# Kernel tuning notes

Hardware: AMD Instinct MI355X
Metric: run time of the kernel (lower is better)

## Reference

```python
import jax, jax.numpy as jnp
import numpy as np

B, C, L, H, W = 8, 64, 32, 64, 64

def setup_inputs() -> dict:
    key = jax.random.key(0)
    k1, k2, k3, k4, k5 = jax.random.split(key, 5)
    inpt = jax.random.normal(k1, (B, C, L, H, W), dtype=jnp.float32)
    # 1x1x1 conv kernels collapse to per-channel vectors
    theta_w = jax.random.normal(k2, (C,), dtype=jnp.float32) * 0.1  # Conv3d(c,1,1) weight
    g_w = jax.random.normal(k3, (C,), dtype=jnp.float32) * 0.1      # Conv3d(c,1,1) weight
    h_w = jax.random.normal(k4, (C,), dtype=jnp.float32) * 0.1      # Conv3d(1,c,1) weight
    h_b = jax.random.normal(k5, (C,), dtype=jnp.float32) * 0.1      # Conv3d(1,c,1) bias
    return {"inpt": inpt, "theta_w": theta_w, "g_w": g_w, "h_w": h_w, "h_b": h_b}

def reference(inpt, theta_w, g_w, h_w, h_b):
    b, c, l, h, w = inpt.shape
    # theta/g: 1x1x1 convs c->1 == channel contraction
    t = jnp.einsum('bclhw,c->blhw', inpt, theta_w).reshape(b, -1)  # (b, N)
    g = jnp.einsum('bclhw,c->blhw', inpt, g_w).reshape(b, -1)      # (b, N)
    # outer product t[b,1,N]*g[b,N,1] followed by AvgPool1d(N) over last axis
    # == g scaled by mean(t); skip the O(N^2) intermediate entirely
    mt = jnp.mean(t, axis=1, keepdims=True)                        # (b, 1)
    x = (g * mt).reshape(b, 1, l, h, w)
    # h: 1x1x1 conv 1->c with bias
    y = x * h_w[None, :, None, None, None] + h_b[None, :, None, None, None]
    return inpt + y
```

## Files before the change

kernel.cpp:

```cpp
#include <hip/hip_runtime.h>

#define BB 8
#define CC 64
#define NSP 131072
#define N4 32768
#define CHUNKS 128

__global__ __launch_bounds__(256) void k1_gpart(
    const float* __restrict__ inpt, const float* __restrict__ theta_w,
    const float* __restrict__ g_w, float* __restrict__ g_out,
    float* __restrict__ partials, int write_g)
{
    int blk = blockIdx.x;
    int b = blk >> 7;
    int n4 = ((blk & 127) << 8) + threadIdx.x;
    const float4* base = reinterpret_cast<const float4*>(inpt)
                         + (((size_t)b) << 21) + n4;

    float4 t4 = make_float4(0.f, 0.f, 0.f, 0.f);
    float4 g4 = make_float4(0.f, 0.f, 0.f, 0.f);
    #pragma unroll 8
    for (int c = 0; c < CC; ++c) {
        float4 x = base[((size_t)c) << 15];
        float tw = theta_w[c];
        float gw = g_w[c];
        t4.x = fmaf(x.x, tw, t4.x); t4.y = fmaf(x.y, tw, t4.y);
        t4.z = fmaf(x.z, tw, t4.z); t4.w = fmaf(x.w, tw, t4.w);
        g4.x = fmaf(x.x, gw, g4.x); g4.y = fmaf(x.y, gw, g4.y);
        g4.z = fmaf(x.z, gw, g4.z); g4.w = fmaf(x.w, gw, g4.w);
    }
    if (write_g)
        reinterpret_cast<float4*>(g_out)[(((size_t)b) << 15) + n4] = g4;

    float t = (t4.x + t4.y) + (t4.z + t4.w);
    #pragma unroll
    for (int off = 32; off > 0; off >>= 1) t += __shfl_down(t, off);
    __shared__ float red[4];
    int wid = threadIdx.x >> 6;
    if ((threadIdx.x & 63) == 0) red[wid] = t;
    __syncthreads();
    if (threadIdx.x == 0) partials[blk] = (red[0] + red[1]) + (red[2] + red[3]);
}

__global__ __launch_bounds__(512) void k2_mt(
    const float* __restrict__ partials, float* __restrict__ mt)
{
    int b = threadIdx.x >> 6;
    int lane = threadIdx.x & 63;
    float v = partials[(b << 7) + lane] + partials[(b << 7) + 64 + lane];
    #pragma unroll
    for (int off = 32; off > 0; off >>= 1) v += __shfl_down(v, off);
    if (lane == 0) mt[b] = v * (1.0f / (float)NSP);
}

__global__ __launch_bounds__(256) void k3_stream(
    const float* __restrict__ inpt, const float* __restrict__ g,
    const float* __restrict__ mt, const float* __restrict__ h_w,
    const float* __restrict__ h_b, float* __restrict__ out)
{
    size_t i4 = (size_t)blockIdx.x * 256 + threadIdx.x;
    int bc = (int)(i4 >> 15);
    int b = bc >> 6, c = bc & 63;
    float4 x  = reinterpret_cast<const float4*>(inpt)[i4];
    float4 gv = reinterpret_cast<const float4*>(g)[(((size_t)b) << 15) + (i4 & 32767)];
    float s  = mt[b] * h_w[c];
    float hb = h_b[c];
    float4 o;
    o.x = fmaf(gv.x, s, x.x + hb);
    o.y = fmaf(gv.y, s, x.y + hb);
    o.z = fmaf(gv.z, s, x.z + hb);
    o.w = fmaf(gv.w, s, x.w + hb);
    reinterpret_cast<float4*>(out)[i4] = o;
}

__global__ __launch_bounds__(256) void k3_reg(
    const float* __restrict__ inpt, const float* __restrict__ g_w,
    const float* __restrict__ mt, const float* __restrict__ h_w,
    const float* __restrict__ h_b, float* __restrict__ out)
{
    size_t idx = (size_t)blockIdx.x * 256 + threadIdx.x;
    int b = (int)(idx >> 17);
    size_t n = idx & (NSP - 1);
    const float* base = inpt + (((size_t)b) * CC) * NSP + n;
    float vals[CC];
    float gacc = 0.f;
    #pragma unroll
    for (int c = 0; c < CC; ++c) {
        vals[c] = base[((size_t)c) << 17];
        gacc = fmaf(vals[c], g_w[c], gacc);
    }
    float s = gacc * mt[b];
    float* obase = out + (((size_t)b) * CC) * NSP + n;
    #pragma unroll
    for (int c = 0; c < CC; ++c)
        obase[((size_t)c) << 17] = fmaf(s, h_w[c], vals[c] + h_b[c]);
}

extern "C" void kernel_launch(void* const* d_in, const int* in_sizes, int n_in,
                              void* d_out, int out_size, void* d_ws, size_t ws_size,
                              hipStream_t stream)
{
    const float* inpt    = (const float*)d_in[0];
    const float* theta_w = (const float*)d_in[1];
    const float* g_w     = (const float*)d_in[2];
    const float* h_w     = (const float*)d_in[3];
    const float* h_b     = (const float*)d_in[4];
    float* out = (float*)d_out;

    const size_t g_bytes   = (size_t)BB * NSP * sizeof(float);
    const size_t need_full = g_bytes + 8192;
    char* ws = (char*)d_ws;

    if (ws_size >= need_full) {
        float* g        = (float*)ws;
        float* partials = (float*)(ws + g_bytes);
        float* mt       = (float*)(ws + g_bytes + 4096);
        hipLaunchKernelGGL(k1_gpart, dim3(BB * CHUNKS), dim3(256), 0, stream,
                           inpt, theta_w, g_w, g, partials, 1);
        hipLaunchKernelGGL(k2_mt, dim3(1), dim3(512), 0, stream, partials, mt);
        hipLaunchKernelGGL(k3_stream, dim3((BB * CC * N4) / 256), dim3(256), 0, stream,
                           inpt, g, mt, h_w, h_b, out);
    } else {
        float* partials = (float*)ws;
        float* mt       = (float*)(ws + 4096);
        hipLaunchKernelGGL(k1_gpart, dim3(BB * CHUNKS), dim3(256), 0, stream,
                           inpt, theta_w, g_w, nullptr, partials, 0);
        hipLaunchKernelGGL(k2_mt, dim3(1), dim3(512), 0, stream, partials, mt);
        hipLaunchKernelGGL(k3_reg, dim3((BB * NSP) / 256), dim3(256), 0, stream,
                           inpt, g_w, mt, h_w, h_b, out);
    }
}
```

Measured before the change: 151.3 us.

## Reduce per-channel sums first and fuse g computation into output pass

The first kernel now computes plain per-(batch, channel) sums over contiguous spans, and theta weighting is applied later in the tiny reduction kernel, since mean(t) equals the sum over channels of theta times each channel mean. The g intermediate buffer is gone: the output kernel always recomputes g in registers from all 64 channels and uses nontemporal stores. This removes the g write and read-back and gives the first pass contiguous reads. In exchange, the final pass does strided per-thread loads across 64 channels and needs many registers.

```diff
diff --git a/kernel.cpp b/kernel.cpp
--- a/kernel.cpp
+++ b/kernel.cpp
@@ -4,76 +4,47 @@
 #define CC 64
 #define NSP 131072
 #define N4 32768
-#define CHUNKS 128
+#define QPB 8
+#define NPART (BB * CC * QPB)
 
-__global__ __launch_bounds__(256) void k1_gpart(
-    const float* __restrict__ inpt, const float* __restrict__ theta_w,
-    const float* __restrict__ g_w, float* __restrict__ g_out,
-    float* __restrict__ partials, int write_g)
+__global__ __launch_bounds__(256) void k1_sum(
+    const float* __restrict__ inpt, float* __restrict__ partials)
 {
     int blk = blockIdx.x;
-    int b = blk >> 7;
-    int n4 = ((blk & 127) << 8) + threadIdx.x;
+    int bc = blk >> 3, q = blk & 7;
     const float4* base = reinterpret_cast<const float4*>(inpt)
-                         + (((size_t)b) << 21) + n4;
-
-    float4 t4 = make_float4(0.f, 0.f, 0.f, 0.f);
-    float4 g4 = make_float4(0.f, 0.f, 0.f, 0.f);
-    #pragma unroll 8
-    for (int c = 0; c < CC; ++c) {
-        float4 x = base[((size_t)c) << 15];
-        float tw = theta_w[c];
-        float gw = g_w[c];
-        t4.x = fmaf(x.x, tw, t4.x); t4.y = fmaf(x.y, tw, t4.y);
-        t4.z = fmaf(x.z, tw, t4.z); t4.w = fmaf(x.w, tw, t4.w);
-        g4.x = fmaf(x.x, gw, g4.x); g4.y = fmaf(x.y, gw, g4.y);
-        g4.z = fmaf(x.z, gw, g4.z); g4.w = fmaf(x.w, gw, g4.w);
+                         + (((size_t)bc) << 15) + (q << 12);
+    float4 s4 = make_float4(0.f, 0.f, 0.f, 0.f);
+    #pragma unroll
+    for (int i = 0; i < 16; ++i) {
+        float4 x = base[i * 256 + threadIdx.x];
+        s4.x += x.x; s4.y += x.y; s4.z += x.z; s4.w += x.w;
     }
-    if (write_g)
-        reinterpret_cast<float4*>(g_out)[(((size_t)b) << 15) + n4] = g4;
-
-    float t = (t4.x + t4.y) + (t4.z + t4.w);
+    float s = (s4.x + s4.y) + (s4.z + s4.w);
     #pragma unroll
-    for (int off = 32; off > 0; off >>= 1) t += __shfl_down(t, off);
+    for (int off = 32; off > 0; off >>= 1) s += __shfl_down(s, off);
     __shared__ float red[4];
     int wid = threadIdx.x >> 6;
-    if ((threadIdx.x & 63) == 0) red[wid] = t;
+    if ((threadIdx.x & 63) == 0) red[wid] = s;
     __syncthreads();
     if (threadIdx.x == 0) partials[blk] = (red[0] + red[1]) + (red[2] + red[3]);
 }
 
 __global__ __launch_bounds__(512) void k2_mt(
-    const float* __restrict__ partials, float* __restrict__ mt)
+    const float* __restrict__ partials, const float* __restrict__ theta_w,
+    float* __restrict__ mt)
 {
     int b = threadIdx.x >> 6;
-    int lane = threadIdx.x & 63;
-    float v = partials[(b << 7) + lane] + partials[(b << 7) + 64 + lane];
+    int c = threadIdx.x & 63;
+    const float* p = partials + (((b << 6) | c) << 3);
+    float v = ((p[0] + p[1]) + (p[2] + p[3])) + ((p[4] + p[5]) + (p[6] + p[7]));
+    v *= theta_w[c];
     #pragma unroll
     for (int off = 32; off > 0; off >>= 1) v += __shfl_down(v, off);
-    if (lane == 0) mt[b] = v * (1.0f / (float)NSP);
+    if (c == 0) mt[b] = v * (1.0f / (float)NSP);
 }
 
-__global__ __launch_bounds__(256) void k3_stream(
-    const float* __restrict__ inpt, const float* __restrict__ g,
-    const float* __restrict__ mt, const float* __restrict__ h_w,
-    const float* __restrict__ h_b, float* __restrict__ out)
-{
-    size_t i4 = (size_t)blockIdx.x * 256 + threadIdx.x;
-    int bc = (int)(i4 >> 15);
-    int b = bc >> 6, c = bc & 63;
-    float4 x  = reinterpret_cast<const float4*>(inpt)[i4];
-    float4 gv = reinterpret_cast<const float4*>(g)[(((size_t)b) << 15) + (i4 & 32767)];
-    float s  = mt[b] * h_w[c];
-    float hb = h_b[c];
-    float4 o;
-    o.x = fmaf(gv.x, s, x.x + hb);
-    o.y = fmaf(gv.y, s, x.y + hb);
-    o.z = fmaf(gv.z, s, x.z + hb);
-    o.w = fmaf(gv.w, s, x.w + hb);
-    reinterpret_cast<float4*>(out)[i4] = o;
-}
-
-__global__ __launch_bounds__(256) void k3_reg(
+__global__ __launch_bounds__(256) void k3_fused(
     const float* __restrict__ inpt, const float* __restrict__ g_w,
     const float* __restrict__ mt, const float* __restrict__ h_w,
     const float* __restrict__ h_b, float* __restrict__ out)
@@ -81,7 +52,8 @@
     size_t idx = (size_t)blockIdx.x * 256 + threadIdx.x;
     int b = (int)(idx >> 17);
     size_t n = idx & (NSP - 1);
-    const float* base = inpt + (((size_t)b) * CC) * NSP + n;
+    const float* base = inpt + ((((size_t)b) << 6) << 17) + n;
+
     float vals[CC];
     float gacc = 0.f;
     #pragma unroll
@@ -90,10 +62,12 @@
         gacc = fmaf(vals[c], g_w[c], gacc);
     }
     float s = gacc * mt[b];
-    float* obase = out + (((size_t)b) * CC) * NSP + n;
+    float* obase = out + ((((size_t)b) << 6) << 17) + n;
     #pragma unroll
-    for (int c = 0; c < CC; ++c)
-        obase[((size_t)c) << 17] = fmaf(s, h_w[c], vals[c] + h_b[c]);
+    for (int c = 0; c < CC; ++c) {
+        float o = fmaf(s, h_w[c], vals[c] + h_b[c]);
+        __builtin_nontemporal_store(o, obase + (((size_t)c) << 17));
+    }
 }
 
 extern "C" void kernel_launch(void* const* d_in, const int* in_sizes, int n_in,
@@ -107,26 +81,14 @@
     const float* h_b     = (const float*)d_in[4];
     float* out = (float*)d_out;
 
-    const size_t g_bytes   = (size_t)BB * NSP * sizeof(float);
-    const size_t need_full = g_bytes + 8192;
     char* ws = (char*)d_ws;
+    float* partials = (float*)ws;
+    float* mt       = (float*)(ws + NPART * sizeof(float));
 
-    if (ws_size >= need_full) {
-        float* g        = (float*)ws;
-        float* partials = (float*)(ws + g_bytes);
-        float* mt       = (float*)(ws + g_bytes + 4096);
-        hipLaunchKernelGGL(k1_gpart, dim3(BB * CHUNKS), dim3(256), 0, stream,
-                           inpt, theta_w, g_w, g, partials, 1);
-        hipLaunchKernelGGL(k2_mt, dim3(1), dim3(512), 0, stream, partials, mt);
-        hipLaunchKernelGGL(k3_stream, dim3((BB * CC * N4) / 256), dim3(256), 0, stream,
-                           inpt, g, mt, h_w, h_b, out);
-    } else {
-        float* partials = (float*)ws;
-        float* mt       = (float*)(ws + 4096);
-        hipLaunchKernelGGL(k1_gpart, dim3(BB * CHUNKS), dim3(256), 0, stream,
-                           inpt, theta_w, g_w, nullptr, partials, 0);
-        hipLaunchKernelGGL(k2_mt, dim3(1), dim3(512), 0, stream, partials, mt);
-        hipLaunchKernelGGL(k3_reg, dim3((BB * NSP) / 256), dim3(256), 0, stream,
-                           inpt, g_w, mt, h_w, h_b, out);
-    }
+    hipLaunchKernelGGL(k1_sum, dim3(NPART), dim3(256), 0, stream,
+                       inpt, partials);
+    hipLaunchKernelGGL(k2_mt, dim3(1), dim3(512), 0, stream,
+                       partials, theta_w, mt);
+    hipLaunchKernelGGL(k3_fused, dim3((BB * NSP) / 256), dim3(256), 0, stream,
+                       inpt, g_w, mt, h_w, h_b, out);
 }
```

Measured after the change: 128.8 us. -14.9%, faster.
